# Performance work log

Hardware: AMD Instinct MI355X
Metric: run time of the kernel (lower is better)

The kernel has to match this reference:

```python
import jax, jax.numpy as jnp
import numpy as np

D = 448  # state_dim == input_dim == output_dim

def _param(key, shape):
    # matches torch.rand(shape) * 0.1 + 0.001
    return jax.random.uniform(key, shape, dtype=jnp.float32) * 0.1 + 0.001

def setup_inputs() -> dict:
    key = jax.random.key(0)
    ks = jax.random.split(key, 9)
    x = jax.random.normal(ks[0], (8, 4096, D), dtype=jnp.float32)
    return {
        "x": x,
        "W_q": _param(ks[1], (D, D)),
        "W_k": _param(ks[2], (D, D)),
        "W_v": _param(ks[3], (D, D)),
        "W_o": _param(ks[4], (D, D)),
        "SSM_A": _param(ks[5], (D, D)),
        "SSM_B": _param(ks[6], (D, D)),
        "SSM_C": _param(ks[7], (D, D)),
    }

def reference(x, W_q, W_k, W_v, W_o, SSM_A, SSM_B, SSM_C):
    # seq_len=4096 > threshold=256 -> quadratic SSM path.
    # structured_processing's einsum 'bsd,dd->bsd' multiplies elementwise by
    # the diagonal of the matrix; the block loop is redundant, so we apply the
    # diagonal scale over the whole sequence in one fused op.
    q = jnp.einsum('bsi,id->bsd', x, W_q)
    k = jnp.einsum('bsi,id->bsd', x, W_k)
    v = jnp.einsum('bsi,id->bsd', x, W_v)
    ssm = (q * jnp.diagonal(SSM_A)
           + k * jnp.diagonal(SSM_B)
           + v * jnp.diagonal(SSM_C))
    # dropout is identity in eval mode
    return jnp.einsum('bsd,do->bso', ssm, W_o)
```

## Files before the change

### kernel.cpp

```cpp
#include <hip/hip_runtime.h>
#include <hip/hip_bf16.h>

#define DDIM 448
#define NSTEP 14

typedef __hip_bfloat16 bf16;
typedef __attribute__((ext_vector_type(8))) short short8;
typedef __attribute__((ext_vector_type(4))) float f32x4;

__device__ __forceinline__ short bf_bits(float f) {
    bf16 h = __float2bfloat16(f);
    return *reinterpret_cast<short*>(&h);
}

__device__ __forceinline__ void async16(const bf16* g, bf16* l) {
    __builtin_amdgcn_global_load_lds(
        (const __attribute__((address_space(1))) void*)g,
        (__attribute__((address_space(3))) void*)l, 16, 0, 0);
}

__global__ __launch_bounds__(256) void prep_wc(
    const float* __restrict__ Wq, const float* __restrict__ Wk,
    const float* __restrict__ Wv, const float* __restrict__ Wo,
    const float* __restrict__ Ad, const float* __restrict__ Bd,
    const float* __restrict__ Cd, bf16* __restrict__ WcT)
{
    __shared__ __align__(16) bf16 As[64 * 32];
    __shared__ __align__(16) bf16 Bs[64 * 32];
    __shared__ float da[DDIM], db[DDIM], dc[DDIM];

    const int tid  = threadIdx.x;
    const int i0   = blockIdx.x * 64;
    const int o0   = blockIdx.y * 64;
    const int lane = tid & 63;
    const int wid  = tid >> 6;
    const int wm   = wid >> 1, wn = wid & 1;
    const int m_   = lane & 15, kq = lane >> 4;

    for (int d = tid; d < DDIM; d += 256) {
        da[d] = Ad[d * DDIM + d];
        db[d] = Bd[d * DDIM + d];
        dc[d] = Cd[d * DDIM + d];
    }

    const int dr  = tid >> 3;
    const int oc8 = (tid & 7) * 8;
    const int ir  = tid >> 2;
    const int dc8 = (tid & 3) * 8;

    f32x4 acc[2][2] = {};

    f32x4 w0 = *(const f32x4*)(Wo + dr * DDIM + o0 + oc8);
    f32x4 w1 = *(const f32x4*)(Wo + dr * DDIM + o0 + oc8 + 4);
    f32x4 q0 = *(const f32x4*)(Wq + (i0 + ir) * DDIM + dc8);
    f32x4 q1 = *(const f32x4*)(Wq + (i0 + ir) * DDIM + dc8 + 4);
    f32x4 t0 = *(const f32x4*)(Wk + (i0 + ir) * DDIM + dc8);
    f32x4 t1 = *(const f32x4*)(Wk + (i0 + ir) * DDIM + dc8 + 4);
    f32x4 v0 = *(const f32x4*)(Wv + (i0 + ir) * DDIM + dc8);
    f32x4 v1 = *(const f32x4*)(Wv + (i0 + ir) * DDIM + dc8 + 4);

    for (int k0 = 0; k0 < DDIM; k0 += 32) {
        __syncthreads();
        #pragma unroll
        for (int j = 0; j < 4; ++j) {
            As[(oc8 + j) * 32 + dr]     = __float2bfloat16(w0[j]);
            As[(oc8 + 4 + j) * 32 + dr] = __float2bfloat16(w1[j]);
        }
        short8 e;
        #pragma unroll
        for (int j = 0; j < 4; ++j) {
            e[j]     = bf_bits(q0[j] * da[k0 + dc8 + j]
                             + t0[j] * db[k0 + dc8 + j]
                             + v0[j] * dc[k0 + dc8 + j]);
            e[j + 4] = bf_bits(q1[j] * da[k0 + dc8 + 4 + j]
                             + t1[j] * db[k0 + dc8 + 4 + j]
                             + v1[j] * dc[k0 + dc8 + 4 + j]);
        }
        *(short8*)&Bs[ir * 32 + dc8] = e;
        __syncthreads();

        const int kn = (k0 + 32 < DDIM) ? k0 + 32 : 0;
        w0 = *(const f32x4*)(Wo + (kn + dr) * DDIM + o0 + oc8);
        w1 = *(const f32x4*)(Wo + (kn + dr) * DDIM + o0 + oc8 + 4);
        q0 = *(const f32x4*)(Wq + (i0 + ir) * DDIM + kn + dc8);
        q1 = *(const f32x4*)(Wq + (i0 + ir) * DDIM + kn + dc8 + 4);
        t0 = *(const f32x4*)(Wk + (i0 + ir) * DDIM + kn + dc8);
        t1 = *(const f32x4*)(Wk + (i0 + ir) * DDIM + kn + dc8 + 4);
        v0 = *(const f32x4*)(Wv + (i0 + ir) * DDIM + kn + dc8);
        v1 = *(const f32x4*)(Wv + (i0 + ir) * DDIM + kn + dc8 + 4);

        short8 af[2], bfr[2];
        #pragma unroll
        for (int mi = 0; mi < 2; ++mi)
            af[mi] = *(const short8*)&As[(wm * 32 + mi * 16 + m_) * 32 + kq * 8];
        #pragma unroll
        for (int ni = 0; ni < 2; ++ni)
            bfr[ni] = *(const short8*)&Bs[(wn * 32 + ni * 16 + m_) * 32 + kq * 8];
        #pragma unroll
        for (int mi = 0; mi < 2; ++mi)
            #pragma unroll
            for (int ni = 0; ni < 2; ++ni)
                acc[mi][ni] = __builtin_amdgcn_mfma_f32_16x16x32_bf16(
                    af[mi], bfr[ni], acc[mi][ni], 0, 0, 0);
    }

    #pragma unroll
    for (int mi = 0; mi < 2; ++mi)
        #pragma unroll
        for (int ni = 0; ni < 2; ++ni) {
            const int o = o0 + wm * 32 + mi * 16 + kq * 4;
            const int i = i0 + wn * 32 + ni * 16 + m_;
            #pragma unroll
            for (int r = 0; r < 4; ++r)
                WcT[(o + r) * DDIM + i] = __float2bfloat16(acc[mi][ni][r]);
        }
}

__global__ __launch_bounds__(256, 2) void gemm_xwc(
    const float* __restrict__ X, const bf16* __restrict__ WcT,
    float* __restrict__ out)
{
    __shared__ __align__(16) char smem[65536];

    const int tid  = threadIdx.x;
    const int lane = tid & 63;
    const int wid  = tid >> 6;
    const int m_   = lane & 15;
    const int kq   = lane >> 4;
    const int row0 = blockIdx.x * 64;

    const int ar = tid >> 2;
    const int ac = (tid & 3) * 8;
    const float* agp = X + (row0 + ar) * DDIM + ac;

    const int lrow = lane >> 2;
    const int lcol = (lane & 3) * 8;
    const bf16* bgp = WcT + (wid * 112 + lrow) * DDIM + lcol;

    f32x4 acc[4][7] = {};

    f32x4 a0 = *(const f32x4*)(agp);
    f32x4 a1 = *(const f32x4*)(agp + 4);
    __builtin_amdgcn_sched_barrier(0);
    {
        bf16* B0 = (bf16*)(smem + 8192);
        #pragma unroll
        for (int j = 0; j < 7; ++j)
            async16(bgp + j * 16 * DDIM, B0 + (wid * 7 + j) * 16 * 32);
    }
    __builtin_amdgcn_sched_barrier(0);
    {
        bf16* A0 = (bf16*)smem;
        short8 w;
        #pragma unroll
        for (int j = 0; j < 4; ++j) {
            w[j] = bf_bits(a0[j]); w[j + 4] = bf_bits(a1[j]);
        }
        *(short8*)&A0[ar * 32 + ac] = w;
    }
    a0 = *(const f32x4*)(agp + 32);
    a1 = *(const f32x4*)(agp + 36);
    asm volatile("s_waitcnt lgkmcnt(0)" ::: "memory");
    __builtin_amdgcn_s_barrier();

    for (int s = 0; s < NSTEP; ++s) {
        const int cur = s & 1, nxt = cur ^ 1;
        const bf16* Ac = (const bf16*)(smem + (cur << 12));
        const bf16* Bc = (const bf16*)(smem + 8192 + cur * 28672);

        if (s + 1 < NSTEP) {
            asm volatile("s_waitcnt vmcnt(2)" ::: "memory");
        } else {
            asm volatile("s_waitcnt vmcnt(0)" ::: "memory");
        }

        short8 af[4], bfr[7];
        #pragma unroll
        for (int mi = 0; mi < 4; ++mi)
            af[mi] = *(const short8*)&Ac[(mi * 16 + m_) * 32 + kq * 8];
        #pragma unroll
        for (int ni = 0; ni < 7; ++ni)
            bfr[ni] = *(const short8*)&Bc[(wid * 112 + ni * 16 + m_) * 32 + kq * 8];

        if (s + 1 < NSTEP) {
            bf16* An = (bf16*)(smem + (nxt << 12));
            bf16* Bn = (bf16*)(smem + 8192 + nxt * 28672);
            short8 w;
            #pragma unroll
            for (int j = 0; j < 4; ++j) {
                w[j] = bf_bits(a0[j]); w[j + 4] = bf_bits(a1[j]);
            }
            *(short8*)&An[ar * 32 + ac] = w;
            const int kn = (s + 1) * 32;
            #pragma unroll
            for (int j = 0; j < 7; ++j)
                async16(bgp + j * 16 * DDIM + kn, Bn + (wid * 7 + j) * 16 * 32);
            __builtin_amdgcn_sched_barrier(0);
            if (s + 2 < NSTEP) {
                const int k2 = (s + 2) * 32;
                a0 = *(const f32x4*)(agp + k2);
                a1 = *(const f32x4*)(agp + k2 + 4);
            }
        }

        #pragma unroll
        for (int mi = 0; mi < 4; ++mi)
            #pragma unroll
            for (int ni = 0; ni < 7; ++ni)
                acc[mi][ni] = __builtin_amdgcn_mfma_f32_16x16x32_bf16(
                    af[mi], bfr[ni], acc[mi][ni], 0, 0, 0);

        asm volatile("s_waitcnt lgkmcnt(0)" ::: "memory");
        __builtin_amdgcn_s_barrier();
    }

    float* Cb = (float*)(smem + 8192);
    const int erow = tid >> 4;
    const int ec0  = tid & 15;
    #pragma unroll
    for (int t = 0; t < 4; ++t) {
        #pragma unroll
        for (int ni = 0; ni < 7; ++ni) {
            const int col = wid * 112 + ni * 16 + m_;
            #pragma unroll
            for (int r = 0; r < 4; ++r)
                Cb[(kq * 4 + r) * 452 + col] = acc[t][ni][r];
        }
        asm volatile("s_waitcnt lgkmcnt(0)" ::: "memory");
        __builtin_amdgcn_s_barrier();
        float* dst = out + (row0 + t * 16) * DDIM;
        #pragma unroll
        for (int j = 0; j < 7; ++j)
            *(f32x4*)(dst + erow * DDIM + (ec0 + j * 16) * 4) =
                *(const f32x4*)(Cb + erow * 452 + (ec0 + j * 16) * 4);
        asm volatile("s_waitcnt lgkmcnt(0)" ::: "memory");
        __builtin_amdgcn_s_barrier();
    }
}

extern "C" void kernel_launch(void* const* d_in, const int* in_sizes, int n_in,
                              void* d_out, int out_size, void* d_ws, size_t ws_size,
                              hipStream_t stream) {
    const float* x  = (const float*)d_in[0];
    const float* Wq = (const float*)d_in[1];
    const float* Wk = (const float*)d_in[2];
    const float* Wv = (const float*)d_in[3];
    const float* Wo = (const float*)d_in[4];
    const float* Ad = (const float*)d_in[5];
    const float* Bd = (const float*)d_in[6];
    const float* Cd = (const float*)d_in[7];

    bf16*  WcT = (bf16*)d_ws;
    float* out = (float*)d_out;

    const int M = in_sizes[0] / DDIM;

    prep_wc<<<dim3(7, 7), 256, 0, stream>>>(Wq, Wk, Wv, Wo, Ad, Bd, Cd, WcT);
    gemm_xwc<<<M / 64, 256, 0, stream>>>(x, WcT, out);
}
```

Measured before the change: 157.4 us.

## Store combined weight in K-tiled layout and move waits to end of step

The prep kernel now writes the combined bf16 weight in k-tiles of 32 columns, each tile stored contiguously as [o][32]. The GEMM's B-tile async loads can then read fully contiguous 512-element chunks per wave instead of strided rows. The main loop is also reordered: next-stage B and A loads are issued before the current LDS reads and MFMAs, and the vmcnt wait moves to the end of each step. This aims to improve global load coalescing and overlap, but the correctness of the vmcnt counting now depends on the exact order in which loads are issued.

```diff
diff --git a/kernel.cpp b/kernel.cpp
--- a/kernel.cpp
+++ b/kernel.cpp
@@ -23,7 +23,7 @@
     const float* __restrict__ Wq, const float* __restrict__ Wk,
     const float* __restrict__ Wv, const float* __restrict__ Wo,
     const float* __restrict__ Ad, const float* __restrict__ Bd,
-    const float* __restrict__ Cd, bf16* __restrict__ WcT)
+    const float* __restrict__ Cd, bf16* __restrict__ Wt)
 {
     __shared__ __align__(16) bf16 As[64 * 32];
     __shared__ __align__(16) bf16 Bs[64 * 32];
@@ -110,14 +110,15 @@
         for (int ni = 0; ni < 2; ++ni) {
             const int o = o0 + wm * 32 + mi * 16 + kq * 4;
             const int i = i0 + wn * 32 + ni * 16 + m_;
+            bf16* dst = Wt + (i >> 5) * (DDIM * 32) + (i & 31);
             #pragma unroll
             for (int r = 0; r < 4; ++r)
-                WcT[(o + r) * DDIM + i] = __float2bfloat16(acc[mi][ni][r]);
+                dst[(o + r) * 32] = __float2bfloat16(acc[mi][ni][r]);
         }
 }
 
 __global__ __launch_bounds__(256, 2) void gemm_xwc(
-    const float* __restrict__ X, const bf16* __restrict__ WcT,
+    const float* __restrict__ X, const bf16* __restrict__ Wt,
     float* __restrict__ out)
 {
     __shared__ __align__(16) char smem[65536];
@@ -133,22 +134,12 @@
     const int ac = (tid & 3) * 8;
     const float* agp = X + (row0 + ar) * DDIM + ac;
 
-    const int lrow = lane >> 2;
-    const int lcol = (lane & 3) * 8;
-    const bf16* bgp = WcT + (wid * 112 + lrow) * DDIM + lcol;
+    const bf16* bgp = Wt + wid * 7 * 512 + lane * 8;
 
     f32x4 acc[4][7] = {};
 
     f32x4 a0 = *(const f32x4*)(agp);
     f32x4 a1 = *(const f32x4*)(agp + 4);
-    __builtin_amdgcn_sched_barrier(0);
-    {
-        bf16* B0 = (bf16*)(smem + 8192);
-        #pragma unroll
-        for (int j = 0; j < 7; ++j)
-            async16(bgp + j * 16 * DDIM, B0 + (wid * 7 + j) * 16 * 32);
-    }
-    __builtin_amdgcn_sched_barrier(0);
     {
         bf16* A0 = (bf16*)smem;
         short8 w;
@@ -158,50 +149,49 @@
         }
         *(short8*)&A0[ar * 32 + ac] = w;
     }
+    {
+        bf16* B0 = (bf16*)(smem + 8192);
+        #pragma unroll
+        for (int j = 0; j < 7; ++j)
+            async16(bgp + j * 512, B0 + (wid * 7 + j) * 512);
+    }
     a0 = *(const f32x4*)(agp + 32);
     a1 = *(const f32x4*)(agp + 36);
+    asm volatile("s_waitcnt vmcnt(2)" ::: "memory");
     asm volatile("s_waitcnt lgkmcnt(0)" ::: "memory");
     __builtin_amdgcn_s_barrier();
 
     for (int s = 0; s < NSTEP; ++s) {
-        const int cur = s & 1, nxt = cur ^ 1;
-        const bf16* Ac = (const bf16*)(smem + (cur << 12));
-        const bf16* Bc = (const bf16*)(smem + 8192 + cur * 28672);
+        const bf16* Ac = (const bf16*)(smem + ((s & 1) << 12));
+        const bf16* Bc = (const bf16*)(smem + 8192 + (s & 1) * 28672);
 
         if (s + 1 < NSTEP) {
-            asm volatile("s_waitcnt vmcnt(2)" ::: "memory");
-        } else {
-            asm volatile("s_waitcnt vmcnt(0)" ::: "memory");
-        }
-
-        short8 af[4], bfr[7];
-        #pragma unroll
-        for (int mi = 0; mi < 4; ++mi)
-            af[mi] = *(const short8*)&Ac[(mi * 16 + m_) * 32 + kq * 8];
-        #pragma unroll
-        for (int ni = 0; ni < 7; ++ni)
-            bfr[ni] = *(const short8*)&Bc[(wid * 112 + ni * 16 + m_) * 32 + kq * 8];
-
-        if (s + 1 < NSTEP) {
-            bf16* An = (bf16*)(smem + (nxt << 12));
-            bf16* Bn = (bf16*)(smem + 8192 + nxt * 28672);
+            bf16* Bn = (bf16*)(smem + 8192 + ((s + 1) & 1) * 28672);
+            const bf16* bsrc = bgp + (s + 1) * (DDIM * 32);
+            #pragma unroll
+            for (int j = 0; j < 7; ++j)
+                async16(bsrc + j * 512, Bn + (wid * 7 + j) * 512);
+            bf16* An = (bf16*)(smem + (((s + 1) & 1) << 12));
             short8 w;
             #pragma unroll
             for (int j = 0; j < 4; ++j) {
                 w[j] = bf_bits(a0[j]); w[j + 4] = bf_bits(a1[j]);
             }
             *(short8*)&An[ar * 32 + ac] = w;
-            const int kn = (s + 1) * 32;
-            #pragma unroll
-            for (int j = 0; j < 7; ++j)
-                async16(bgp + j * 16 * DDIM + kn, Bn + (wid * 7 + j) * 16 * 32);
-            __builtin_amdgcn_sched_barrier(0);
-            if (s + 2 < NSTEP) {
-                const int k2 = (s + 2) * 32;
-                a0 = *(const f32x4*)(agp + k2);
-                a1 = *(const f32x4*)(agp + k2 + 4);
-            }
-        }
+        }
+        if (s + 2 < NSTEP) {
+            const int k2 = (s + 2) * 32;
+            a0 = *(const f32x4*)(agp + k2);
+            a1 = *(const f32x4*)(agp + k2 + 4);
+        }
+
+        short8 af[4], bfr[7];
+        #pragma unroll
+        for (int mi = 0; mi < 4; ++mi)
+            af[mi] = *(const short8*)&Ac[(mi * 16 + m_) * 32 + kq * 8];
+        #pragma unroll
+        for (int ni = 0; ni < 7; ++ni)
+            bfr[ni] = *(const short8*)&Bc[(wid * 112 + ni * 16 + m_) * 32 + kq * 8];
 
         #pragma unroll
         for (int mi = 0; mi < 4; ++mi)
@@ -210,6 +200,11 @@
                 acc[mi][ni] = __builtin_amdgcn_mfma_f32_16x16x32_bf16(
                     af[mi], bfr[ni], acc[mi][ni], 0, 0, 0);
 
+        if (s + 2 < NSTEP) {
+            asm volatile("s_waitcnt vmcnt(2)" ::: "memory");
+        } else {
+            asm volatile("s_waitcnt vmcnt(0)" ::: "memory");
+        }
         asm volatile("s_waitcnt lgkmcnt(0)" ::: "memory");
         __builtin_amdgcn_s_barrier();
     }
@@ -250,11 +245,11 @@
     const float* Bd = (const float*)d_in[6];
     const float* Cd = (const float*)d_in[7];
 
-    bf16*  WcT = (bf16*)d_ws;
+    bf16*  Wt  = (bf16*)d_ws;
     float* out = (float*)d_out;
 
     const int M = in_sizes[0] / DDIM;
 
-    prep_wc<<<dim3(7, 7), 256, 0, stream>>>(Wq, Wk, Wv, Wo, Ad, Bd, Cd, WcT);
-    gemm_xwc<<<M / 64, 256, 0, stream>>>(x, WcT, out);
-}
+    prep_wc<<<dim3(7, 7), 256, 0, stream>>>(Wq, Wk, Wv, Wo, Ad, Bd, Cd, Wt);
+    gemm_xwc<<<M / 64, 256, 0, stream>>>(x, Wt, out);
+}
```

Result: faster. 145.5 us (-7.5%).
